# Kernel optimization log

Hardware: AMD Instinct MI355X
Metric: run time of the kernel (lower is better)

Reference implementation:

```python
import jax, jax.numpy as jnp
import numpy as np

B, S, CIN = 16384, 24, 10
NH, DK, DM = 16, 8, 256
DV = DM // NH  # 16
EPS = 1e-5
T_POS = 1000.0


def _ln(x, g, b):
    mu = jnp.mean(x, axis=-1, keepdims=True)
    var = jnp.mean((x - mu) ** 2, axis=-1, keepdims=True)
    return (x - mu) * jax.lax.rsqrt(var + EPS) * g + b


def _bn(x, g, b, m, v):
    # eval-mode BatchNorm1d over channel (last) dim
    return (x - m) * jax.lax.rsqrt(v + EPS) * g + b


def setup_inputs() -> dict:
    key = jax.random.key(0)
    ks = jax.random.split(key, 16)
    x = jax.random.normal(ks[0], (B, S, CIN + 1), dtype=jnp.float32)
    pos = jax.random.uniform(ks[1], (B, S), dtype=jnp.float32) * 365.0
    x = x.at[:, :, 0].set(pos)
    w = lambda k, shp, s=0.05: (jax.random.normal(k, shp, dtype=jnp.float32) * s)
    d = {
        'x': x,
        'ln1_g': jnp.ones((CIN,), jnp.float32), 'ln1_b': jnp.zeros((CIN,), jnp.float32),
        'conv_w': w(ks[2], (DM, CIN)), 'conv_b': jnp.zeros((DM,), jnp.float32),
        'bn1_g': jnp.ones((DM,), jnp.float32), 'bn1_b': jnp.zeros((DM,), jnp.float32),
        'bn1_m': jnp.zeros((DM,), jnp.float32), 'bn1_v': jnp.ones((DM,), jnp.float32),
        'Q': w(ks[3], (NH, DK), float(np.sqrt(2.0 / DK))),
        'Wk': w(ks[4], (NH * DK, DM), float(np.sqrt(2.0 / DK))), 'bk': jnp.zeros((NH * DK,), jnp.float32),
        'W1': w(ks[5], (128, 256)), 'b1': jnp.zeros((128,), jnp.float32),
        'bn2_g': jnp.ones((128,), jnp.float32), 'bn2_b': jnp.zeros((128,), jnp.float32),
        'bn2_m': jnp.zeros((128,), jnp.float32), 'bn2_v': jnp.ones((128,), jnp.float32),
        'oln_g': jnp.ones((128,), jnp.float32), 'oln_b': jnp.zeros((128,), jnp.float32),
        'Wd1': w(ks[6], (64, 128)), 'bd1': jnp.zeros((64,), jnp.float32),
        'bnd1_g': jnp.ones((64,), jnp.float32), 'bnd1_b': jnp.zeros((64,), jnp.float32),
        'bnd1_m': jnp.zeros((64,), jnp.float32), 'bnd1_v': jnp.ones((64,), jnp.float32),
        'Wd2': w(ks[7], (32, 64)), 'bd2': jnp.zeros((32,), jnp.float32),
        'bnd2_g': jnp.ones((32,), jnp.float32), 'bnd2_b': jnp.zeros((32,), jnp.float32),
        'bnd2_m': jnp.zeros((32,), jnp.float32), 'bnd2_v': jnp.ones((32,), jnp.float32),
        'Wd3': w(ks[8], (20, 32)), 'bd3': jnp.zeros((20,), jnp.float32),
    }
    return d


def reference(x, ln1_g, ln1_b, conv_w, conv_b, bn1_g, bn1_b, bn1_m, bn1_v,
              Q, Wk, bk, W1, b1, bn2_g, bn2_b, bn2_m, bn2_v, oln_g, oln_b,
              Wd1, bd1, bnd1_g, bnd1_b, bnd1_m, bnd1_v,
              Wd2, bd2, bnd2_g, bnd2_b, bnd2_m, bnd2_v, Wd3, bd3):
    pos = x[:, :, 0]            # (B, S) positions
    feat = x[:, :, 1:]          # (B, S, CIN)
    feat = _ln(feat, ln1_g, ln1_b)
    # inconv: 1x1 Conv1d == per-timestep Linear, then eval BatchNorm1d over channels
    h = jnp.einsum('bsc,dc->bsd', feat, conv_w) + conv_b
    h = _bn(h, bn1_g, bn1_b, bn1_m, bn1_v)
    # sinusoid positional encoding, interleaved sin/cos
    div = jnp.exp(jnp.arange(0, DM, 2, dtype=jnp.float32) * (-np.log(T_POS) / DM))  # (DM/2,)
    ang = pos[:, :, None] * div                                   # (B, S, DM/2)
    pe = jnp.stack([jnp.sin(ang), jnp.cos(ang)], axis=-1).reshape(pos.shape[0], pos.shape[1], DM)
    e = h + pe                                                    # (B, S, DM)
    # LTAE multi-head attention with shared learned query
    k = jnp.einsum('bsd,hkd->bshk', e, Wk.reshape(NH, DK, DM)) + bk.reshape(NH, DK)
    logits = jnp.einsum('hk,bshk->bhs', Q, k) / np.sqrt(DK)
    attn = jax.nn.softmax(logits, axis=-1)                        # (B, NH, S); dropout=eval
    v = e.reshape(e.shape[0], e.shape[1], NH, DV)                 # head-chunked values
    o = jnp.einsum('bhs,bshc->bhc', attn, v).reshape(e.shape[0], NH * DV)  # (B, 256)
    # MLP3: Linear(256,128) + BN + ReLU, then dropout(eval) + LayerNorm
    m = jax.nn.relu(_bn(o @ W1.T + b1, bn2_g, bn2_b, bn2_m, bn2_v))
    m = _ln(m, oln_g, oln_b)
    # decoder: [128,64,32,20]
    d1 = jax.nn.relu(_bn(m @ Wd1.T + bd1, bnd1_g, bnd1_b, bnd1_m, bnd1_v))
    d2 = jax.nn.relu(_bn(d1 @ Wd2.T + bd2, bnd2_g, bnd2_b, bnd2_m, bnd2_v))
    out = d2 @ Wd3.T + bd3                                        # (B, 20)
    return out
```

## Files before the change

kernel.cpp:

```cpp
#include <hip/hip_runtime.h>
#include <hip/hip_bf16.h>


typedef __attribute__((ext_vector_type(8))) short bf16x8;
typedef __attribute__((ext_vector_type(4))) float f32x4;

#define EPS 1e-5f
#define INV_SQRT8 0.35355339059327373f
#define KDIV (-0.07785768972392256f)
#define INV2PI 0.15915494309189535f
#define LOG2E 1.4426950408889634f

__device__ __forceinline__ unsigned short f2bf(float f){
  union { float f; unsigned u; } v; v.f = f;
  unsigned r = v.u + 0x7FFFu + ((v.u >> 16) & 1u);
  return (unsigned short)(r >> 16);
}
__device__ __forceinline__ float bf2f(unsigned short h){
  union { unsigned u; float f; } v; v.u = ((unsigned)h) << 16; return v.f;
}
__device__ __forceinline__ float asf(unsigned u){
  union { unsigned u; float f; } v; v.u = u; return v.f;
}
__device__ __forceinline__ unsigned pk2bf(float lo, float hi){
  __hip_bfloat162 h2 = __float22bfloat162_rn(make_float2(lo, hi));
  return *reinterpret_cast<unsigned*>(&h2);
}

__global__ __launch_bounds__(256) void k0_pre(
    const float* __restrict__ conv_w, const float* __restrict__ conv_b,
    const float* __restrict__ bn1_g, const float* __restrict__ bn1_b,
    const float* __restrict__ bn1_m, const float* __restrict__ bn1_v,
    const float* __restrict__ Q, const float* __restrict__ Wk,
    const float* __restrict__ bk,
    const float* __restrict__ W1, const float* __restrict__ b1,
    const float* __restrict__ bn2_g, const float* __restrict__ bn2_b,
    const float* __restrict__ bn2_m, const float* __restrict__ bn2_v,
    const float* __restrict__ oln_g, const float* __restrict__ oln_b,
    const float* __restrict__ Wd1, const float* __restrict__ bd1,
    const float* __restrict__ bnd1_g, const float* __restrict__ bnd1_b,
    const float* __restrict__ bnd1_m, const float* __restrict__ bnd1_v,
    const float* __restrict__ Wd2, const float* __restrict__ bd2,
    const float* __restrict__ bnd2_g, const float* __restrict__ bnd2_b,
    const float* __restrict__ bnd2_m, const float* __restrict__ bnd2_v,
    const float* __restrict__ Wd3,
    unsigned short* __restrict__ wqF, unsigned short* __restrict__ w1F,
    unsigned short* __restrict__ wd1F, unsigned short* __restrict__ wd2F,
    unsigned short* __restrict__ wd3F,
    float* __restrict__ convwT, float* __restrict__ convbE,
    float* __restrict__ biasq, float* __restrict__ b1E,
    float* __restrict__ bd1E, float* __restrict__ bd2E)
{
  __shared__ float redL[256];
  const int t = threadIdx.x;
  const int bid = blockIdx.x;

  if (bid < 64){
    for (int e = bid*512 + t; e < bid*512 + 512; e += 256){
      int j = e & 7, lj = (e >> 3) & 63, kc = (e >> 9) & 7, nt = (e >> 12) & 7;
      int n = nt*16 + (lj & 15);
      int k = kc*32 + ((lj >> 4) << 3) + j;
      float s2 = bn2_g[n] * rsqrtf(bn2_v[n] + EPS);
      w1F[e] = f2bf(W1[n*256 + k] * s2);
    }
  } else if (bid < 68){
    int base = (bid - 64)*2048;
    #pragma unroll 4
    for (int it = 0; it < 8; ++it){
      int e = base + it*256 + t;
      int j = e & 7, lj = (e >> 3) & 63, kc = (e >> 9) & 3, nt = (e >> 11) & 3;
      int n = nt*16 + (lj & 15);
      int k = kc*32 + ((lj >> 4) << 3) + j;
      float sd = bnd1_g[n] * rsqrtf(bnd1_v[n] + EPS);
      wd1F[e] = f2bf(Wd1[n*128 + k] * sd * oln_g[k]);
    }
  } else if (bid == 68){
    #pragma unroll 4
    for (int it = 0; it < 8; ++it){
      int e = it*256 + t;
      int j = e & 7, lj = (e >> 3) & 63, kc = (e >> 9) & 1, nt = (e >> 10) & 1;
      int n = nt*16 + (lj & 15);
      int k = kc*32 + ((lj >> 4) << 3) + j;
      float sd = bnd2_g[n] * rsqrtf(bnd2_v[n] + EPS);
      wd2F[e] = f2bf(Wd2[n*64 + k] * sd);
    }
  } else if (bid == 69){
    #pragma unroll
    for (int it = 0; it < 4; ++it){
      int e = it*256 + t;
      int j = e & 7, lj = (e >> 3) & 63, nt = (e >> 9) & 1;
      int n = nt*16 + (lj & 15);
      int k = ((lj >> 4) << 3) + j;
      float v = (n < 20) ? Wd3[n*32 + k] : 0.f;
      wd3F[e] = f2bf(v);
    }
  } else if (bid == 70){
    #pragma unroll 4
    for (int it = 0; it < 16; ++it){
      int e = it*256 + t;
      int j = e & 7, lj = (e >> 3) & 63, kc = (e >> 9) & 7;
      int h = lj & 15;
      int dd = kc*32 + ((lj >> 4) << 3) + j;
      float acc = 0.f;
      #pragma unroll
      for (int kk = 0; kk < 8; ++kk)
        acc += Q[h*8+kk] * Wk[(h*8+kk)*256 + dd];
      wqF[e] = f2bf(acc * INV_SQRT8);
    }
  } else if (bid == 71){
    __shared__ float wqL[16*257];
    __shared__ float coefL[256*12];
    __shared__ float QL[128];
    __shared__ float bkL[128];
    wqF[4096 + t] = 0; wqF[4096 + 256 + t] = 0;
    if (t < 128){ QL[t] = Q[t]; bkL[t] = bk[t]; }
    __syncthreads();
    {
      const int d = t;
      float s1 = bn1_g[d] * rsqrtf(bn1_v[d] + EPS);
      #pragma unroll
      for (int c = 0; c < 10; ++c) coefL[d*12 + c] = conv_w[d*10 + c] * s1;
      coefL[d*12 + 10] = conv_b[d]*s1 + bn1_b[d] - bn1_m[d]*s1;
      coefL[d*12 + 11] = 0.f;
      #pragma unroll 4
      for (int h = 0; h < 16; ++h){
        float acc = 0.f;
        #pragma unroll
        for (int kk = 0; kk < 8; ++kk)
          acc += QL[h*8+kk] * Wk[(h*8+kk)*256 + d];
        wqL[h*257 + d] = acc;
      }
    }
    __syncthreads();
    if (t < 176){
      int h = t / 11, cc = t - h*11;
      const float* wq = wqL + h*257;
      float acc = 0.f;
      #pragma unroll 4
      for (int d2 = 0; d2 < 256; ++d2)
        acc += coefL[d2*12 + cc] * wq[d2];
      acc *= INV_SQRT8;
      if (cc < 10){
        int lane = (cc < 8) ? h : (16 + h);
        int j = cc & 7;
        wqF[4096 + lane*8 + j] = f2bf(acc);
      } else {
        float qb = 0.f;
        #pragma unroll
        for (int kk = 0; kk < 8; ++kk) qb += QL[h*8+kk]*bkL[h*8+kk];
        biasq[h] = acc + qb * INV_SQRT8;
      }
    }
  } else if (bid == 72){
    #pragma unroll
    for (int it = 0; it < 10; ++it){
      int e = it*256 + t;
      int c = e >> 8, d = e & 255;
      float s1 = bn1_g[d] * rsqrtf(bn1_v[d] + EPS);
      convwT[e] = conv_w[d*10 + c] * s1;
    }
  } else if (bid == 73){
    {
      int d = t;
      float s1 = bn1_g[d] * rsqrtf(bn1_v[d] + EPS);
      convbE[d] = conv_b[d]*s1 + bn1_b[d] - bn1_m[d]*s1;
    }
    if (t < 128){
      float s2 = bn2_g[t] * rsqrtf(bn2_v[t] + EPS);
      b1E[t] = b1[t]*s2 + bn2_b[t] - bn2_m[t]*s2;
    }
    if (t < 32){
      float sd = bnd2_g[t] * rsqrtf(bnd2_v[t] + EPS);
      bd2E[t] = bd2[t]*sd + bnd2_b[t] - bnd2_m[t]*sd;
    }
  } else {
    int n = t >> 2, si = t & 3;
    float acc = 0.f;
    #pragma unroll 8
    for (int i2 = 0; i2 < 32; ++i2){
      int i = si*32 + i2;
      acc += oln_b[i] * Wd1[n*128 + i];
    }
    redL[t] = acc;
    __syncthreads();
    if (t < 64){
      float sd = bnd1_g[t] * rsqrtf(bnd1_v[t] + EPS);
      float a = redL[4*t] + redL[4*t+1] + redL[4*t+2] + redL[4*t+3];
      bd1E[t] = bd1[t]*sd + bnd1_b[t] - bnd1_m[t]*sd + a*sd;
    }
  }
}

__global__ __launch_bounds__(256, 4) void k1_attn(
    const float* __restrict__ x, const float* __restrict__ ln1_g,
    const float* __restrict__ ln1_b,
    const unsigned short* __restrict__ wqF, const float* __restrict__ convwT,
    const float* __restrict__ convbE, const float* __restrict__ biasq,
    unsigned short* __restrict__ o_frag)
{
  __shared__ __align__(16) unsigned short peR[48*264];
  __shared__ __align__(16) float attnF[32*24];
  __shared__ __align__(16) unsigned short featn[48*16];
  __shared__ __align__(16) float divL[128];
  __shared__ __align__(16) float xL[536];
  float* gL = xL;

  const int t = threadIdx.x;
  const int b0 = blockIdx.x * 2;
  const int w = t >> 6, l = t & 63;

  if (t < 132)
    *(float4*)(xL + t*4) = *(const float4*)(x + (size_t)b0*264 + t*4);
  else if (t < 134)
    *(float4*)(xL + 528 + (t-132)*4) = make_float4(0.f,0.f,0.f,0.f);
  if (t < 128) divL[t] = exp2f((float)t * KDIV) * INV2PI;
  __syncthreads();

  {
    const int g = (l >> 4) & 3, rlo = l & 15;
    #pragma unroll
    for (int it = 0; it < 6; ++it){
      int combo = it*4 + w;
      int mt = combo >> 3, kc = combo & 7;
      int row = mt*16 + rlo;
      int run = kc*4 + g;
      float p = xL[row*11];
      unsigned pk[4];
      #pragma unroll
      for (int q = 0; q < 4; ++q){
        float fr = __builtin_amdgcn_fractf(p * divL[run*4 + q]);
        pk[q] = pk2bf(__builtin_amdgcn_sinf(fr), __builtin_amdgcn_cosf(fr));
      }
      *(uint4*)(peR + row*264 + run*8) = make_uint4(pk[0], pk[1], pk[2], pk[3]);
    }
  }
  if (w == 3 && l < 48){
    const float* xr = xL + l*11;
    float f[10]; float mu = 0.f;
    #pragma unroll
    for (int c = 0; c < 10; ++c){ f[c] = xr[1+c]; mu += f[c]; }
    mu *= 0.1f;
    float var = 0.f;
    #pragma unroll
    for (int c = 0; c < 10; ++c){ float dv = f[c]-mu; var += dv*dv; }
    var *= 0.1f;
    float rs = rsqrtf(var + EPS);
    float fn[10];
    #pragma unroll
    for (int c = 0; c < 10; ++c) fn[c] = (f[c]-mu)*rs*ln1_g[c] + ln1_b[c];
    #pragma unroll
    for (int q = 0; q < 5; ++q)
      *(unsigned*)(featn + l*16 + 2*q) = pk2bf(fn[2*q], fn[2*q+1]);
    #pragma unroll
    for (int z = 0; z < 3; ++z)
      *(unsigned*)(featn + l*16 + 10 + 2*z) = 0u;
  }
  __syncthreads();

  const int m = l & 15, g = l >> 4;
  if (w < 3){
    const int mt = w;
    f32x4 acc = {0.f,0.f,0.f,0.f};
    #pragma unroll
    for (int kc = 0; kc < 8; ++kc){
      bf16x8 a = *(const bf16x8*)(peR + (mt*16 + m)*264 + kc*32 + g*8);
      bf16x8 b = *(const bf16x8*)(wqF + ((size_t)(kc*64 + l))*8);
      acc = __builtin_amdgcn_mfma_f32_16x16x32_bf16(a, b, acc, 0, 0, 0);
    }
    {
      const unsigned short* ap = (g < 2) ? (featn + (mt*16 + m)*16 + g*8)
                                         : (const unsigned short*)(xL + 528);
      bf16x8 a = *(const bf16x8*)ap;
      bf16x8 b = *(const bf16x8*)(wqF + ((size_t)(8*64 + l))*8);
      acc = __builtin_amdgcn_mfma_f32_16x16x32_bf16(a, b, acc, 0, 0, 0);
    }
    float bq = biasq[m];
    #pragma unroll
    for (int reg = 0; reg < 4; ++reg){
      int row = mt*16 + g*4 + reg;
      int bb = row >= 24; int s = row - bb*24;
      attnF[(bb*16+m)*24 + s] = acc[reg] + bq;
    }
  }
  __syncthreads();

  {
    const int bh = t >> 3, ln = t & 7;
    float* L = attnF + bh*24;
    float v0 = L[ln], v1 = L[ln+8], v2 = L[ln+16];
    float mx = fmaxf(fmaxf(v0, v1), v2);
    mx = fmaxf(mx, __shfl_xor(mx, 1, 64));
    mx = fmaxf(mx, __shfl_xor(mx, 2, 64));
    mx = fmaxf(mx, __shfl_xor(mx, 4, 64));
    float p0 = exp2f((v0-mx)*LOG2E);
    float p1 = exp2f((v1-mx)*LOG2E);
    float p2 = exp2f((v2-mx)*LOG2E);
    float sm = p0 + p1 + p2;
    sm += __shfl_xor(sm, 1, 64);
    sm += __shfl_xor(sm, 2, 64);
    sm += __shfl_xor(sm, 4, 64);
    float inv = 1.f / sm;
    L[ln] = p0*inv; L[ln+8] = p1*inv; L[ln+16] = p2*inv;
  }
  __syncthreads();

  if (w < 2){
    const int bb = w;
    const int q = g;
    union { bf16x8 v; unsigned u[4]; } aF;
    if (q < 3){
      const float* ap = attnF + (bb*16 + m)*24 + q*8;
      float4 a0 = *(const float4*)ap;
      float4 a1 = *(const float4*)(ap + 4);
      aF.u[0] = pk2bf(a0.x, a0.y); aF.u[1] = pk2bf(a0.z, a0.w);
      aF.u[2] = pk2bf(a1.x, a1.y); aF.u[3] = pk2bf(a1.z, a1.w);
    } else {
      aF.u[0] = 0u; aF.u[1] = 0u; aF.u[2] = 0u; aF.u[3] = 0u;
    }
    union { bf16x8 v; unsigned short s[8]; } bF;
    #pragma unroll
    for (int j = 0; j < 8; ++j){
      int s = q*8 + j;
      bF.s[j] = (s < 24) ? featn[(bb*24 + s)*16 + m] : (unsigned short)0;
    }
    f32x4 z = {0.f,0.f,0.f,0.f};
    f32x4 ga = __builtin_amdgcn_mfma_f32_16x16x32_bf16(aF.v, bF.v, z, 0,0,0);
    if (m < 12){
      #pragma unroll
      for (int reg = 0; reg < 4; ++reg){
        int h = q*4 + reg;
        gL[(bb*16+h)*12 + m] = ga[reg];
      }
    }
  }
  __syncthreads();

  {
    const int bb = t >> 7, dp = t & 127;
    const int d0 = dp*2, h = dp >> 3;
    float2 o2 = *(const float2*)(convbE + d0);
    const float* gp = gL + (bb*16+h)*12;
    #pragma unroll
    for (int c = 0; c < 10; ++c){
      float2 cw = *(const float2*)(convwT + c*256 + d0);
      o2.x += cw.x * gp[c];
      o2.y += cw.y * gp[c];
    }
    float A[24];
    {
      const float* Ab = attnF + (bb*16+h)*24;
      #pragma unroll
      for (int q4 = 0; q4 < 6; ++q4)
        *(float4*)(A + q4*4) = *(const float4*)(Ab + q4*4);
    }
    const unsigned short* pr = peR + bb*24*264 + d0;
    #pragma unroll
    for (int s = 0; s < 24; ++s){
      unsigned u = *(const unsigned*)(pr + s*264);
      o2.x += A[s] * asf(u << 16);
      o2.y += A[s] * asf(u & 0xFFFF0000u);
    }
    const int row = b0 + bb;
    const int rt = row >> 4, mm = row & 15;
    const int kc = d0 >> 5, gg = (d0 >> 3) & 3, j = d0 & 7;
    *(unsigned*)(o_frag + ((size_t)((rt*8+kc)*64 + gg*16 + mm))*8 + j)
        = pk2bf(o2.x, o2.y);
  }
}

__global__ __launch_bounds__(256, 4) void k2_mlp(
    const unsigned short* __restrict__ o_frag,
    const unsigned short* __restrict__ w1F, const float* __restrict__ b1E,
    const unsigned short* __restrict__ wd1F, const float* __restrict__ bd1E,
    const unsigned short* __restrict__ wd2F, const float* __restrict__ bd2E,
    const unsigned short* __restrict__ wd3F, const float* __restrict__ bd3,
    float* __restrict__ out)
{
  __shared__ float mL[16*132];
  __shared__ unsigned short mh[16*136];
  __shared__ unsigned short d1L[16*72];
  __shared__ unsigned short d2L[16*40];
  __shared__ float redL[64];
  __shared__ float stats[32];

  const int t = threadIdx.x;
  const int w = t >> 6, l = t & 63;
  const size_t rowBase = (size_t)blockIdx.x * 16;
  const int rt = blockIdx.x;
  const int g8  = (l >> 4) << 3;
  const int c15 = l & 15;

  {
    f32x4 acc[2];
    { f32x4 z = {0.f,0.f,0.f,0.f}; acc[0] = z; acc[1] = z; }
    #pragma unroll
    for (int kc = 0; kc < 8; ++kc){
      bf16x8 a = *(const bf16x8*)(o_frag + ((size_t)((rt*8+kc)*64 + l))*8);
      #pragma unroll
      for (int n2 = 0; n2 < 2; ++n2){
        int nt = 2*w + n2;
        bf16x8 b = *(const bf16x8*)(w1F + ((size_t)((nt*8+kc)*64 + l))*8);
        acc[n2] = __builtin_amdgcn_mfma_f32_16x16x32_bf16(a, b, acc[n2], 0,0,0);
      }
    }
    #pragma unroll
    for (int n2 = 0; n2 < 2; ++n2){
      int col = (2*w + n2)*16 + c15;
      float be = b1E[col];
      #pragma unroll
      for (int reg = 0; reg < 4; ++reg){
        int row = ((l>>4)<<2) + reg;
        mL[row*132 + col] = fmaxf(acc[n2][reg] + be, 0.f);
      }
    }
  }
  __syncthreads();

  if (t < 32){
    const float* R = mL + (t>>1)*132 + (t&1)*64;
    float s = 0.f, q = 0.f;
    for (int k = 0; k < 64; ++k){ float v = R[k]; s += v; q += v*v; }
    redL[t*2] = s; redL[t*2+1] = q;
  }
  __syncthreads();
  if (t < 16){
    float s = redL[4*t] + redL[4*t+2];
    float q = redL[4*t+1] + redL[4*t+3];
    float mu = s * (1.f/128.f);
    float var = q * (1.f/128.f) - mu*mu;
    stats[2*t] = mu; stats[2*t+1] = rsqrtf(var + EPS);
  }
  __syncthreads();

  {
    int r = t >> 4, run = t & 15;
    float mu = stats[2*r], rs = stats[2*r+1];
    const float* R = mL + r*132 + run*8;
    unsigned pk[4];
    #pragma unroll
    for (int q = 0; q < 4; ++q)
      pk[q] = pk2bf((R[2*q]-mu)*rs, (R[2*q+1]-mu)*rs);
    *(uint4*)(mh + r*136 + run*8) = make_uint4(pk[0], pk[1], pk[2], pk[3]);
  }
  __syncthreads();

  {
    const int nt = w;
    f32x4 acc = {0.f,0.f,0.f,0.f};
    #pragma unroll
    for (int kc = 0; kc < 4; ++kc){
      bf16x8 b = *(const bf16x8*)(wd1F + ((size_t)((nt*4+kc)*64 + l))*8);
      bf16x8 a = *(const bf16x8*)(mh + c15*136 + kc*32 + g8);
      acc = __builtin_amdgcn_mfma_f32_16x16x32_bf16(a, b, acc, 0,0,0);
    }
    int col = nt*16 + c15;
    float be = bd1E[col];
    #pragma unroll
    for (int reg = 0; reg < 4; ++reg){
      int row = ((l>>4)<<2) + reg;
      d1L[row*72 + col] = f2bf(fmaxf(acc[reg] + be, 0.f));
    }
  }
  __syncthreads();

  if (w < 2){
    const int nt = w;
    f32x4 acc = {0.f,0.f,0.f,0.f};
    #pragma unroll
    for (int kc = 0; kc < 2; ++kc){
      bf16x8 a = *(const bf16x8*)(d1L + c15*72 + kc*32 + g8);
      bf16x8 b = *(const bf16x8*)(wd2F + ((size_t)((nt*2+kc)*64 + l))*8);
      acc = __builtin_amdgcn_mfma_f32_16x16x32_bf16(a, b, acc, 0,0,0);
    }
    int col = nt*16 + c15;
    float be = bd2E[col];
    #pragma unroll
    for (int reg = 0; reg < 4; ++reg){
      int row = ((l>>4)<<2) + reg;
      d2L[row*40 + col] = f2bf(fmaxf(acc[reg] + be, 0.f));
    }
  }
  __syncthreads();

  if (w < 2){
    const int nt = w;
    bf16x8 a = *(const bf16x8*)(d2L + c15*40 + g8);
    bf16x8 b = *(const bf16x8*)(wd3F + ((size_t)(nt*64 + l))*8);
    f32x4 acc = {0.f,0.f,0.f,0.f};
    acc = __builtin_amdgcn_mfma_f32_16x16x32_bf16(a, b, acc, 0,0,0);
    int col = nt*16 + c15;
    if (col < 20){
      float be = bd3[col];
      #pragma unroll
      for (int reg = 0; reg < 4; ++reg){
        int row = ((l>>4)<<2) + reg;
        out[(rowBase + row)*20 + col] = acc[reg] + be;
      }
    }
  }
}

extern "C" void kernel_launch(void* const* d_in, const int* in_sizes, int n_in,
                              void* d_out, int out_size, void* d_ws, size_t ws_size,
                              hipStream_t stream)
{
  (void)in_sizes; (void)n_in; (void)out_size; (void)ws_size;
  const float* x      = (const float*)d_in[0];
  const float* ln1_g  = (const float*)d_in[1];
  const float* ln1_b  = (const float*)d_in[2];
  const float* conv_w = (const float*)d_in[3];
  const float* conv_b = (const float*)d_in[4];
  const float* bn1_g  = (const float*)d_in[5];
  const float* bn1_b  = (const float*)d_in[6];
  const float* bn1_m  = (const float*)d_in[7];
  const float* bn1_v  = (const float*)d_in[8];
  const float* Q      = (const float*)d_in[9];
  const float* Wk     = (const float*)d_in[10];
  const float* bk     = (const float*)d_in[11];
  const float* W1     = (const float*)d_in[12];
  const float* b1     = (const float*)d_in[13];
  const float* bn2_g  = (const float*)d_in[14];
  const float* bn2_b  = (const float*)d_in[15];
  const float* bn2_m  = (const float*)d_in[16];
  const float* bn2_v  = (const float*)d_in[17];
  const float* oln_g  = (const float*)d_in[18];
  const float* oln_b  = (const float*)d_in[19];
  const float* Wd1    = (const float*)d_in[20];
  const float* bd1    = (const float*)d_in[21];
  const float* bnd1_g = (const float*)d_in[22];
  const float* bnd1_b = (const float*)d_in[23];
  const float* bnd1_m = (const float*)d_in[24];
  const float* bnd1_v = (const float*)d_in[25];
  const float* Wd2    = (const float*)d_in[26];
  const float* bd2    = (const float*)d_in[27];
  const float* bnd2_g = (const float*)d_in[28];
  const float* bnd2_b = (const float*)d_in[29];
  const float* bnd2_m = (const float*)d_in[30];
  const float* bnd2_v = (const float*)d_in[31];
  const float* Wd3    = (const float*)d_in[32];
  const float* bd3    = (const float*)d_in[33];

  char* ws = (char*)d_ws;
  unsigned short* wqF  = (unsigned short*)(ws + 0);
  unsigned short* w1F  = (unsigned short*)(ws + 9216);
  unsigned short* wd1F = (unsigned short*)(ws + 74752);
  unsigned short* wd2F = (unsigned short*)(ws + 91136);
  unsigned short* wd3F = (unsigned short*)(ws + 95232);
  float* convwT = (float*)(ws + 97280);
  float* convbE = (float*)(ws + 107520);
  float* biasq  = (float*)(ws + 108544);
  float* b1E    = (float*)(ws + 108608);
  float* bd1E   = (float*)(ws + 109120);
  float* bd2E   = (float*)(ws + 109376);
  unsigned short* o_frag = (unsigned short*)(ws + 109568);

  hipLaunchKernelGGL(k0_pre, dim3(75), dim3(256), 0, stream,
      conv_w, conv_b, bn1_g, bn1_b, bn1_m, bn1_v, Q, Wk, bk,
      W1, b1, bn2_g, bn2_b, bn2_m, bn2_v, oln_g, oln_b,
      Wd1, bd1, bnd1_g, bnd1_b, bnd1_m, bnd1_v,
      Wd2, bd2, bnd2_g, bnd2_b, bnd2_m, bnd2_v, Wd3,
      wqF, w1F, wd1F, wd2F, wd3F, convwT, convbE, biasq, b1E, bd1E, bd2E);

  hipLaunchKernelGGL(k1_attn, dim3(8192), dim3(256), 0, stream,
      x, ln1_g, ln1_b, wqF, convwT, convbE, biasq, o_frag);

  hipLaunchKernelGGL(k2_mlp, dim3(1024), dim3(256), 0, stream,
      o_frag, w1F, b1E, wd1F, bd1E, wd2F, bd2E, wd3F, bd3, (float*)d_out);
}
```

Before: 183.9 us.

## Use polynomial sin/cos, overlap PE-weighted sum with MFMA, split wq precompute

Replaces the hardware sin/cos transcendental calls for the positional encoding with minimax polynomials on a range-reduced argument. Moves the attention-weighted PE accumulation ahead of a barrier, so waves 0-1 do it while waves 2-3 run the MFMA feature projection, and drops one __syncthreads. Splits the wq fold precompute across four blocks instead of one by launching more k0 blocks. The polynomial approximation may lose some accuracy relative to the hardware sin/cos, which matters little after bf16 rounding.

Result: no change. 186.2 us (+1.3%).

```diff
diff --git a/kernel.cpp b/kernel.cpp
--- a/kernel.cpp
+++ b/kernel.cpp
@@ -10,6 +10,16 @@
 #define KDIV (-0.07785768972392256f)
 #define INV2PI 0.15915494309189535f
 #define LOG2E 1.4426950408889634f
+
+#define SA1 6.2785980f
+#define SA3 -41.0922624f
+#define SA5 77.9146240f
+#define SA7 -56.0414720f
+#define CC0 0.9999973f
+#define CC2 -19.7317952f
+#define CC4 64.6724864f
+#define CC6 -82.3955456f
+#define CC8 45.6261632f
 
 __device__ __forceinline__ unsigned short f2bf(float f){
   union { float f; unsigned u; } v; v.f = f;
@@ -94,10 +104,11 @@
       float v = (n < 20) ? Wd3[n*32 + k] : 0.f;
       wd3F[e] = f2bf(v);
     }
-  } else if (bid == 70){
-    #pragma unroll 4
-    for (int it = 0; it < 16; ++it){
-      int e = it*256 + t;
+  } else if (bid == 70 || bid >= 75){
+    int c0 = (bid == 70) ? 0 : (bid - 74)*4;
+    #pragma unroll
+    for (int i2 = 0; i2 < 4; ++i2){
+      int e = (c0 + i2)*256 + t;
       int j = e & 7, lj = (e >> 3) & 63, kc = (e >> 9) & 7;
       int h = lj & 15;
       int dd = kc*32 + ((lj >> 4) << 3) + j;
@@ -228,8 +239,12 @@
       unsigned pk[4];
       #pragma unroll
       for (int q = 0; q < 4; ++q){
-        float fr = __builtin_amdgcn_fractf(p * divL[run*4 + q]);
-        pk[q] = pk2bf(__builtin_amdgcn_sinf(fr), __builtin_amdgcn_cosf(fr));
+        float f  = p * divL[run*4 + q];
+        float r  = f - __builtin_rintf(f);
+        float s  = r*r;
+        float sp = fmaf(fmaf(fmaf(SA7, s, SA5), s, SA3), s, SA1) * r;
+        float cp = fmaf(fmaf(fmaf(fmaf(CC8, s, CC6), s, CC4), s, CC2), s, CC0);
+        pk[q] = pk2bf(sp, cp);
       }
       *(uint4*)(peR + row*264 + run*8) = make_uint4(pk[0], pk[1], pk[2], pk[3]);
     }
@@ -304,8 +319,8 @@
   }
   __syncthreads();
 
-  if (w < 2){
-    const int bb = w;
+  if (w >= 2){
+    const int bb = w - 2;
     const int q = g;
     union { bf16x8 v; unsigned u[4]; } aF;
     if (q < 3){
@@ -333,34 +348,37 @@
       }
     }
   }
-  __syncthreads();
-
-  {
-    const int bb = t >> 7, dp = t & 127;
-    const int d0 = dp*2, h = dp >> 3;
-    float2 o2 = *(const float2*)(convbE + d0);
-    const float* gp = gL + (bb*16+h)*12;
+
+  const int bb7 = t >> 7, dp = t & 127;
+  const int d0 = dp*2, h7 = dp >> 3;
+  float2 o2; o2.x = 0.f; o2.y = 0.f;
+  {
+    float A[24];
+    const float* Ab = attnF + (bb7*16+h7)*24;
+    #pragma unroll
+    for (int q4 = 0; q4 < 6; ++q4)
+      *(float4*)(A + q4*4) = *(const float4*)(Ab + q4*4);
+    const unsigned short* pr = peR + bb7*24*264 + d0;
+    #pragma unroll
+    for (int s = 0; s < 24; ++s){
+      unsigned u = *(const unsigned*)(pr + s*264);
+      o2.x += A[s] * asf(u << 16);
+      o2.y += A[s] * asf(u & 0xFFFF0000u);
+    }
+  }
+  __syncthreads();
+
+  {
+    float2 cb2 = *(const float2*)(convbE + d0);
+    o2.x += cb2.x; o2.y += cb2.y;
+    const float* gp = gL + (bb7*16+h7)*12;
     #pragma unroll
     for (int c = 0; c < 10; ++c){
       float2 cw = *(const float2*)(convwT + c*256 + d0);
       o2.x += cw.x * gp[c];
       o2.y += cw.y * gp[c];
     }
-    float A[24];
-    {
-      const float* Ab = attnF + (bb*16+h)*24;
-      #pragma unroll
-      for (int q4 = 0; q4 < 6; ++q4)
-        *(float4*)(A + q4*4) = *(const float4*)(Ab + q4*4);
-    }
-    const unsigned short* pr = peR + bb*24*264 + d0;
-    #pragma unroll
-    for (int s = 0; s < 24; ++s){
-      unsigned u = *(const unsigned*)(pr + s*264);
-      o2.x += A[s] * asf(u << 16);
-      o2.y += A[s] * asf(u & 0xFFFF0000u);
-    }
-    const int row = b0 + bb;
+    const int row = b0 + bb7;
     const int rt = row >> 4, mm = row & 15;
     const int kc = d0 >> 5, gg = (d0 >> 3) & 3, j = d0 & 7;
     *(unsigned*)(o_frag + ((size_t)((rt*8+kc)*64 + gg*16 + mm))*8 + j)
@@ -554,7 +572,7 @@
   float* bd2E   = (float*)(ws + 109376);
   unsigned short* o_frag = (unsigned short*)(ws + 109568);
 
-  hipLaunchKernelGGL(k0_pre, dim3(75), dim3(256), 0, stream,
+  hipLaunchKernelGGL(k0_pre, dim3(78), dim3(256), 0, stream,
       conv_w, conv_b, bn1_g, bn1_b, bn1_m, bn1_v, Q, Wk, bk,
       W1, b1, bn2_g, bn2_b, bn2_m, bn2_v, oln_g, oln_b,
       Wd1, bd1, bnd1_g, bnd1_b, bnd1_m, bnd1_v,
```
